# Performance work log

Measured on AMD Instinct MI355X. Metric: run time of the kernel, lower is better.

Reference implementation:

```python
import jax, jax.numpy as jnp
import numpy as np

B, C, CI, H, W = 4, 64, 32, 96, 96  # batch, in_channels, inter_channels, spatial
EPS = 1e-5


def conv1x1(x, w, b):
    # x: [B,Cin,H,W], w: [Cout,Cin], b: [Cout]
    return jnp.einsum('bchw,oc->bohw', x, w) + b[None, :, None, None]


def maxpool2(x):
    b, c, h, w = x.shape
    return x.reshape(b, c, h // 2, 2, w // 2, 2).max(axis=(3, 5))


def setup_inputs() -> dict:
    key = jax.random.key(0)
    ks = jax.random.split(key, 12)
    s = 0.05  # keep unscaled attention logits in a sane range
    return {
        'x': jax.random.normal(ks[0], (B, C, H, W), jnp.float32),
        'feature': jax.random.normal(ks[1], (B, CI, H, W), jnp.float32),
        'g_w': jax.random.normal(ks[2], (C, C), jnp.float32) * s,
        'g_b': jax.random.normal(ks[3], (C,), jnp.float32) * s,
        'theta_w': jax.random.normal(ks[4], (C, C), jnp.float32) * s,
        'theta_b': jax.random.normal(ks[5], (C,), jnp.float32) * s,
        'phi_w': jax.random.normal(ks[6], (C, CI), jnp.float32) * s,
        'phi_b': jax.random.normal(ks[7], (C,), jnp.float32) * s,
        'W_w': jax.random.normal(ks[8], (CI, C), jnp.float32) * s,
        'W_b': jax.random.normal(ks[9], (CI,), jnp.float32) * s,
        'bn_gamma': jax.random.normal(ks[10], (CI,), jnp.float32) * s + 1.0,
        'bn_beta': jax.random.normal(ks[11], (CI,), jnp.float32) * s,
    }


def reference(x, feature, g_w, g_b, theta_w, theta_b, phi_w, phi_b, W_w, W_b, bn_gamma, bn_beta):
    b = x.shape[0]
    # g branch: conv1x1 then 2x2 maxpool -> [B, M, C]
    g_x = maxpool2(conv1x1(x, g_w, g_b)).reshape(b, C, -1).transpose(0, 2, 1)
    # theta: conv1x1 -> [B, N, C]
    theta_x = conv1x1(x, theta_w, theta_b).reshape(b, C, -1).transpose(0, 2, 1)
    # phi on `feature` (inter_channels -> in_channels) then maxpool -> [B, C, M]
    phi_f = maxpool2(conv1x1(feature, phi_w, phi_b)).reshape(b, C, -1)
    # unscaled attention: [B, N, M]
    f = jnp.einsum('bnc,bcm->bnm', theta_x, phi_f)
    f_div_C = jax.nn.softmax(f, axis=-1)
    y = jnp.einsum('bnm,bmc->bnc', f_div_C, g_x)  # [B, N, C]
    y = y.transpose(0, 2, 1).reshape(x.shape)
    z = y + x
    # W: conv1x1 (C -> CI) + BatchNorm2d (training mode, batch stats)
    z = conv1x1(z, W_w, W_b)
    mean = z.mean(axis=(0, 2, 3), keepdims=True)
    var = z.var(axis=(0, 2, 3), keepdims=True)
    z = (z - mean) * jax.lax.rsqrt(var + EPS)
    z = z * bn_gamma[None, :, None, None] + bn_beta[None, :, None, None]
    return z
```

## Files before the change

kernel.cpp:

```cpp
#include <hip/hip_runtime.h>
#include <hip/hip_bf16.h>

typedef __attribute__((ext_vector_type(8))) short short8;
typedef __attribute__((ext_vector_type(4))) float f32x4;
typedef __attribute__((ext_vector_type(4))) _Float16 half4;
typedef __attribute__((ext_vector_type(8))) _Float16 half8;

#define NB 4
#define NN 9216
#define NM 2304

__device__ inline unsigned pk2(float a, float b) {
  __hip_bfloat16 ha = __float2bfloat16(a), hb = __float2bfloat16(b);
  return (unsigned)*(unsigned short*)&ha | ((unsigned)*(unsigned short*)&hb << 16);
}
__device__ inline short8 pack8(const float* v) {
  short8 s;
#pragma unroll
  for (int j = 0; j < 8; ++j) { __hip_bfloat16 h = __float2bfloat16(v[j]); s[j] = *(short*)&h; }
  return s;
}
__device__ inline short8 ldw8(const float* p) {
  float tmp[8];
  *(float4*)&tmp[0] = *(const float4*)p;
  *(float4*)&tmp[4] = *(const float4*)(p + 4);
  return pack8(tmp);
}

__global__ __launch_bounds__(256) void conv_pool_k(
    const float* __restrict__ x, const float* __restrict__ feat,
    const float* __restrict__ tw, const float* __restrict__ tbi,
    const float* __restrict__ gw, const float* __restrict__ gbi,
    const float* __restrict__ pw, const float* __restrict__ pbi,
    __hip_bfloat16* __restrict__ Theta, _Float16* __restrict__ Gcm,
    __hip_bfloat16* __restrict__ PhiT, float* __restrict__ psum) {
  int t = threadIdx.x, wv = t >> 6, lane = t & 63, l15 = lane & 15, q = lane >> 4;
  int b = blockIdx.y, bx = blockIdx.x;
  if (bx == 0 && b == 0 && t < 64) psum[t] = 0.f;
  int jt = bx % 6, rp = bx / 6;
  int i0 = rp * 2, j0 = jt * 16;
  int ntop = i0 * 96 + j0;
  int ot = wv;

  short8 wt[2], wg[2], wp1;
#pragma unroll
  for (int kf = 0; kf < 2; ++kf) {
    wt[kf] = ldw8(tw + (size_t)(ot * 16 + l15) * 64 + kf * 32 + q * 8);
    wg[kf] = ldw8(gw + (size_t)(ot * 16 + l15) * 64 + kf * 32 + q * 8);
  }
  wp1 = ldw8(pw + (size_t)(ot * 16 + l15) * 32 + q * 8);

  short8 bxf[2][2], bff[2];
  {
    float tmp[8];
#pragma unroll
    for (int row = 0; row < 2; ++row) {
#pragma unroll
      for (int kf = 0; kf < 2; ++kf) {
#pragma unroll
        for (int j = 0; j < 8; ++j)
          tmp[j] = x[((size_t)b * 64 + kf * 32 + q * 8 + j) * NN + ntop + row * 96 + l15];
        bxf[row][kf] = pack8(tmp);
      }
#pragma unroll
      for (int j = 0; j < 8; ++j)
        tmp[j] = feat[((size_t)b * 32 + q * 8 + j) * NN + ntop + row * 96 + l15];
      bff[row] = pack8(tmp);
    }
  }

  int m = rp * 48 + ((j0 + l15) >> 1);
  bool em = (l15 & 1) == 0;

#pragma unroll
  for (int row = 0; row < 2; ++row) {
    f32x4 d;
#pragma unroll
    for (int r = 0; r < 4; ++r) d[r] = tbi[ot * 16 + q * 4 + r];
    d = __builtin_amdgcn_mfma_f32_16x16x32_bf16(wt[0], bxf[row][0], d, 0, 0, 0);
    d = __builtin_amdgcn_mfma_f32_16x16x32_bf16(wt[1], bxf[row][1], d, 0, 0, 0);
    size_t base = ((size_t)b * NN + ntop + row * 96 + l15) * 64 + ot * 16 + q * 4;
    *(unsigned*)(Theta + base) = pk2(d[0], d[1]);
    *(unsigned*)(Theta + base + 2) = pk2(d[2], d[3]);
  }
  {
    f32x4 d0, d1;
#pragma unroll
    for (int r = 0; r < 4; ++r) { float bb = gbi[ot * 16 + q * 4 + r]; d0[r] = bb; d1[r] = bb; }
    d0 = __builtin_amdgcn_mfma_f32_16x16x32_bf16(wg[0], bxf[0][0], d0, 0, 0, 0);
    d0 = __builtin_amdgcn_mfma_f32_16x16x32_bf16(wg[1], bxf[0][1], d0, 0, 0, 0);
    d1 = __builtin_amdgcn_mfma_f32_16x16x32_bf16(wg[0], bxf[1][0], d1, 0, 0, 0);
    d1 = __builtin_amdgcn_mfma_f32_16x16x32_bf16(wg[1], bxf[1][1], d1, 0, 0, 0);
    float h[4];
#pragma unroll
    for (int r = 0; r < 4; ++r) {
      float v = fmaxf(d0[r], d1[r]);
      h[r] = fmaxf(v, __shfl_xor(v, 1));
    }
    if (em) {
#pragma unroll
      for (int r = 0; r < 4; ++r)
        Gcm[((size_t)b * 64 + ot * 16 + q * 4 + r) * NM + m] = (_Float16)h[r];
    }
  }
  {
    f32x4 d0, d1;
#pragma unroll
    for (int r = 0; r < 4; ++r) { float bb = pbi[ot * 16 + q * 4 + r]; d0[r] = bb; d1[r] = bb; }
    d0 = __builtin_amdgcn_mfma_f32_16x16x32_bf16(wp1, bff[0], d0, 0, 0, 0);
    d1 = __builtin_amdgcn_mfma_f32_16x16x32_bf16(wp1, bff[1], d1, 0, 0, 0);
    float h[4];
#pragma unroll
    for (int r = 0; r < 4; ++r) {
      float v = fmaxf(d0[r], d1[r]);
      h[r] = fmaxf(v, __shfl_xor(v, 1));
    }
    if (em) {
      size_t base = ((size_t)b * NM + m) * 64 + ot * 16 + q * 4;
      *(unsigned*)(PhiT + base) = pk2(h[0], h[1]);
      *(unsigned*)(PhiT + base + 2) = pk2(h[2], h[3]);
    }
  }
}

__global__ __launch_bounds__(256) void attn_k(
    const __hip_bfloat16* __restrict__ Theta, const __hip_bfloat16* __restrict__ PhiT,
    const _Float16* __restrict__ Gcm, const float* __restrict__ x,
    const float* __restrict__ Ww, const float* __restrict__ Wb,
    float* __restrict__ z2, float* __restrict__ psum) {
  __shared__ union {
    struct {
      __hip_bfloat16 phis[64][72];
      _Float16 gs2[64][72];
    } s;
    __hip_bfloat16 zacc[64][72];
  } u;
  __shared__ float rs[4][64];

  int t = threadIdx.x, wv = t >> 6, lane = t & 63;
  int l15 = lane & 15, q = lane >> 4;
  int b = blockIdx.y;
  int n0 = blockIdx.x * 64, nw = n0 + wv * 16;

  short8 tb[2];
#pragma unroll
  for (int kf = 0; kf < 2; ++kf)
    tb[kf] = *(const short8*)(Theta + ((size_t)b * NN + nw + l15) * 64 + kf * 32 + q * 8);

  f32x4 acc[4];
#pragma unroll
  for (int ct = 0; ct < 4; ++ct) acc[ct] = (f32x4){0.f, 0.f, 0.f, 0.f};
  float rsum = 0.f;

  const __hip_bfloat16* phibase = PhiT + (size_t)b * NM * 64;
  const _Float16* gbase = Gcm + (size_t)b * 64 * NM;

  for (int ck = 0; ck < NM / 64; ++ck) {
    int m0 = ck * 64;
    __syncthreads();
#pragma unroll
    for (int p = 0; p < 2; ++p) {
      int idx = p * 256 + t, r = idx >> 3, seg = idx & 7;
      *(uint4*)&u.s.phis[r][seg * 8] = *(const uint4*)(phibase + (size_t)(m0 + r) * 64 + seg * 8);
    }
#pragma unroll
    for (int p = 0; p < 2; ++p) {
      int idx = p * 256 + t, c = idx >> 3, g = idx & 7;
      int pp = g >> 2, qq = g & 3;
      const _Float16* gc = gbase + (size_t)c * NM + m0 + pp * 32 + qq * 4;
      uint2 lo = *(const uint2*)gc;
      uint2 hi = *(const uint2*)(gc + 16);
      uint4 w; w.x = lo.x; w.y = lo.y; w.z = hi.x; w.w = hi.y;
      *(uint4*)&u.s.gs2[c][g * 8] = w;
    }
    __syncthreads();

    short8 pha[4][2];
#pragma unroll
    for (int tm = 0; tm < 4; ++tm)
#pragma unroll
      for (int kf = 0; kf < 2; ++kf)
        pha[tm][kf] = *(const short8*)&u.s.phis[tm * 16 + l15][kf * 32 + q * 8];
    half8 gv[4][2];
#pragma unroll
    for (int ct = 0; ct < 4; ++ct)
#pragma unroll
      for (int pp = 0; pp < 2; ++pp)
        gv[ct][pp] = *(const half8*)&u.s.gs2[ct * 16 + l15][pp * 32 + q * 8];

    half4 pa[4];
#pragma unroll
    for (int tm = 0; tm < 4; ++tm) {
      f32x4 s = (f32x4){0.f, 0.f, 0.f, 0.f};
      s = __builtin_amdgcn_mfma_f32_16x16x32_bf16(pha[tm][0], tb[0], s, 0, 0, 0);
      s = __builtin_amdgcn_mfma_f32_16x16x32_bf16(pha[tm][1], tb[1], s, 0, 0, 0);
      float e0 = __expf(s[0]), e1 = __expf(s[1]), e2 = __expf(s[2]), e3 = __expf(s[3]);
      rsum += (e0 + e1) + (e2 + e3);
      pa[tm] = (half4){(_Float16)e0, (_Float16)e1, (_Float16)e2, (_Float16)e3};
    }
#pragma unroll
    for (int ct = 0; ct < 4; ++ct)
#pragma unroll
      for (int pp = 0; pp < 2; ++pp) {
        half4 glo = __builtin_shufflevector(gv[ct][pp], gv[ct][pp], 0, 1, 2, 3);
        half4 ghi = __builtin_shufflevector(gv[ct][pp], gv[ct][pp], 4, 5, 6, 7);
        acc[ct] = __builtin_amdgcn_mfma_f32_16x16x16f16(pa[2 * pp], glo, acc[ct], 0, 0, 0);
        acc[ct] = __builtin_amdgcn_mfma_f32_16x16x16f16(pa[2 * pp + 1], ghi, acc[ct], 0, 0, 0);
      }
  }

  float v = rsum;
  v += __shfl_xor(v, 16);
  v += __shfl_xor(v, 32);
  float rinv = 1.0f / v;
  float riv[4];
#pragma unroll
  for (int r = 0; r < 4; ++r) riv[r] = __shfl(rinv, q * 4 + r);

  __syncthreads();

#pragma unroll
  for (int ct = 0; ct < 4; ++ct) {
#pragma unroll
    for (int r = 0; r < 4; ++r) {
      float xv = x[((size_t)b * 64 + ct * 16 + l15) * NN + nw + q * 4 + r];
      u.zacc[wv * 16 + q * 4 + r][ct * 16 + l15] =
          __float2bfloat16(acc[ct][r] * riv[r] + xv);
    }
  }
  __syncthreads();

  short8 wbf[2][2];
#pragma unroll
  for (int ot = 0; ot < 2; ++ot)
#pragma unroll
    for (int kf = 0; kf < 2; ++kf)
      wbf[ot][kf] = ldw8(Ww + (size_t)(ot * 16 + l15) * 64 + kf * 32 + q * 8);
  short8 za0 = *(const short8*)&u.zacc[wv * 16 + l15][q * 8];
  short8 za1 = *(const short8*)&u.zacc[wv * 16 + l15][32 + q * 8];

  f32x4 dd[2];
#pragma unroll
  for (int ot = 0; ot < 2; ++ot) {
    float bias = Wb[ot * 16 + l15];
    f32x4 d = (f32x4){bias, bias, bias, bias};
    d = __builtin_amdgcn_mfma_f32_16x16x32_bf16(za0, wbf[ot][0], d, 0, 0, 0);
    d = __builtin_amdgcn_mfma_f32_16x16x32_bf16(za1, wbf[ot][1], d, 0, 0, 0);
#pragma unroll
    for (int r = 0; r < 4; ++r)
      z2[((size_t)b * NN + nw + q * 4 + r) * 32 + ot * 16 + l15] = d[r];
    dd[ot] = d;
  }

#pragma unroll
  for (int ot = 0; ot < 2; ++ot) {
    float ps = (dd[ot][0] + dd[ot][1]) + (dd[ot][2] + dd[ot][3]);
    float ps2 = dd[ot][0] * dd[ot][0] + dd[ot][1] * dd[ot][1] +
                dd[ot][2] * dd[ot][2] + dd[ot][3] * dd[ot][3];
    ps += __shfl_xor(ps, 16);  ps += __shfl_xor(ps, 32);
    ps2 += __shfl_xor(ps2, 16); ps2 += __shfl_xor(ps2, 32);
    if (lane < 16) {
      rs[wv][ot * 16 + lane] = ps;
      rs[wv][32 + ot * 16 + lane] = ps2;
    }
  }
  __syncthreads();
  if (t < 64) {
    float tot = rs[0][t] + rs[1][t] + rs[2][t] + rs[3][t];
    atomicAdd(&psum[t], tot);
  }
}

__global__ __launch_bounds__(256) void bn_apply(
    const float* __restrict__ z2, const float* __restrict__ psum,
    const float* __restrict__ gamma, const float* __restrict__ beta,
    float* __restrict__ out) {
  __shared__ float ssl[64];
  __shared__ float zt[32][65];
  int t = threadIdx.x, b = blockIdx.y, n0 = blockIdx.x * 64;
  if (t < 32) {
    const float inv = 1.0f / (float)(NB * NN);
    float mean = psum[t] * inv;
    float var = psum[32 + t] * inv - mean * mean;
    float sc = gamma[t] * rsqrtf(var + 1e-5f);
    ssl[t] = sc;
    ssl[32 + t] = beta[t] - mean * sc;
  }
#pragma unroll
  for (int it = 0; it < 2; ++it) {
    int idx = it * 256 + t, r = idx >> 3, seg = idx & 7;
    float4 vv = *(const float4*)(z2 + ((size_t)b * NN + n0 + r) * 32 + seg * 4);
    zt[seg * 4 + 0][r] = vv.x; zt[seg * 4 + 1][r] = vv.y;
    zt[seg * 4 + 2][r] = vv.z; zt[seg * 4 + 3][r] = vv.w;
  }
  __syncthreads();
  int o = t >> 3, nseg = t & 7;
  float sc = ssl[o], sh = ssl[32 + o];
  float4 a, c;
  a.x = zt[o][nseg * 8 + 0] * sc + sh; a.y = zt[o][nseg * 8 + 1] * sc + sh;
  a.z = zt[o][nseg * 8 + 2] * sc + sh; a.w = zt[o][nseg * 8 + 3] * sc + sh;
  c.x = zt[o][nseg * 8 + 4] * sc + sh; c.y = zt[o][nseg * 8 + 5] * sc + sh;
  c.z = zt[o][nseg * 8 + 6] * sc + sh; c.w = zt[o][nseg * 8 + 7] * sc + sh;
  float* po = out + ((size_t)b * 32 + o) * NN + n0 + nseg * 8;
  *(float4*)po = a;
  *(float4*)(po + 4) = c;
}

extern "C" void kernel_launch(void* const* d_in, const int* in_sizes, int n_in,
                              void* d_out, int out_size, void* d_ws, size_t ws_size,
                              hipStream_t stream) {
  const float* x       = (const float*)d_in[0];
  const float* feature = (const float*)d_in[1];
  const float* g_w     = (const float*)d_in[2];
  const float* g_b     = (const float*)d_in[3];
  const float* theta_w = (const float*)d_in[4];
  const float* theta_b = (const float*)d_in[5];
  const float* phi_w   = (const float*)d_in[6];
  const float* phi_b   = (const float*)d_in[7];
  const float* W_w     = (const float*)d_in[8];
  const float* W_b     = (const float*)d_in[9];
  const float* bn_g    = (const float*)d_in[10];
  const float* bn_b    = (const float*)d_in[11];

  char* ws = (char*)d_ws;
  __hip_bfloat16* Theta = (__hip_bfloat16*)(ws);
  _Float16*       Gcm   = (_Float16*)(ws + 4718592);
  __hip_bfloat16* PhiT  = (__hip_bfloat16*)(ws + 5898240);
  float*          z2    = (float*)(ws + 7077888);
  float*          psum  = (float*)(ws + 11796480);

  conv_pool_k<<<dim3(288, NB), dim3(256), 0, stream>>>(
      x, feature, theta_w, theta_b, g_w, g_b, phi_w, phi_b, Theta, Gcm, PhiT, psum);
  attn_k<<<dim3(144, NB), dim3(256), 0, stream>>>(
      Theta, PhiT, Gcm, x, W_w, W_b, z2, psum);
  bn_apply<<<dim3(144, NB), dim3(256), 0, stream>>>(
      z2, psum, bn_g, bn_b, (float*)d_out);
}
```

Measured before the change: 157.9 us.

## Split attention keys across waves and stage conv inputs through LDS

```diff
diff --git a/kernel.cpp b/kernel.cpp
--- a/kernel.cpp
+++ b/kernel.cpp
@@ -4,7 +4,6 @@
 typedef __attribute__((ext_vector_type(8))) short short8;
 typedef __attribute__((ext_vector_type(4))) float f32x4;
 typedef __attribute__((ext_vector_type(4))) _Float16 half4;
-typedef __attribute__((ext_vector_type(8))) _Float16 half8;
 
 #define NB 4
 #define NN 9216
@@ -13,6 +12,9 @@
 __device__ inline unsigned pk2(float a, float b) {
   __hip_bfloat16 ha = __float2bfloat16(a), hb = __float2bfloat16(b);
   return (unsigned)*(unsigned short*)&ha | ((unsigned)*(unsigned short*)&hb << 16);
+}
+__device__ inline float ubf(unsigned u) {
+  unsigned v = u << 16; return *(float*)&v;
 }
 __device__ inline short8 pack8(const float* v) {
   short8 s;
@@ -27,20 +29,42 @@
   return pack8(tmp);
 }
 
-__global__ __launch_bounds__(256) void conv_pool_k(
+__global__ __launch_bounds__(256, 3) void conv_pool_k(
     const float* __restrict__ x, const float* __restrict__ feat,
     const float* __restrict__ tw, const float* __restrict__ tbi,
     const float* __restrict__ gw, const float* __restrict__ gbi,
     const float* __restrict__ pw, const float* __restrict__ pbi,
     __hip_bfloat16* __restrict__ Theta, _Float16* __restrict__ Gcm,
     __hip_bfloat16* __restrict__ PhiT, float* __restrict__ psum) {
+  __shared__ float xs[64][68];
+  __shared__ float fs[64][36];
   int t = threadIdx.x, wv = t >> 6, lane = t & 63, l15 = lane & 15, q = lane >> 4;
   int b = blockIdx.y, bx = blockIdx.x;
   if (bx == 0 && b == 0 && t < 64) psum[t] = 0.f;
-  int jt = bx % 6, rp = bx / 6;
-  int i0 = rp * 2, j0 = jt * 16;
-  int ntop = i0 * 96 + j0;
+  int jt = bx % 3, rp = bx / 3;
+  int i0 = rp * 2, j0 = jt * 32;
   int ot = wv;
+
+  {
+#pragma unroll
+    for (int p = 0; p < 4; ++p) {
+      int idx = p * 256 + t;
+      int c = idx >> 4, s = idx & 15;
+      int row = s >> 3, cl = (s & 7) * 4;
+      float4 v = *(const float4*)(x + ((size_t)b * 64 + c) * NN + (i0 + row) * 96 + j0 + cl);
+      int nl = row * 32 + cl;
+      xs[nl][c] = v.x; xs[nl + 1][c] = v.y; xs[nl + 2][c] = v.z; xs[nl + 3][c] = v.w;
+    }
+#pragma unroll
+    for (int p = 0; p < 2; ++p) {
+      int idx = p * 256 + t;
+      int c = idx >> 4, s = idx & 15;
+      int row = s >> 3, cl = (s & 7) * 4;
+      float4 v = *(const float4*)(feat + ((size_t)b * 32 + c) * NN + (i0 + row) * 96 + j0 + cl);
+      int nl = row * 32 + cl;
+      fs[nl][c] = v.x; fs[nl + 1][c] = v.y; fs[nl + 2][c] = v.z; fs[nl + 3][c] = v.w;
+    }
+  }
 
   short8 wt[2], wg[2], wp1;
 #pragma unroll
@@ -50,47 +74,49 @@
   }
   wp1 = ldw8(pw + (size_t)(ot * 16 + l15) * 32 + q * 8);
 
-  short8 bxf[2][2], bff[2];
+  __syncthreads();
+
+  short8 bxf[4][2], bff[4];
   {
     float tmp[8];
 #pragma unroll
-    for (int row = 0; row < 2; ++row) {
+    for (int tl = 0; tl < 4; ++tl) {
 #pragma unroll
       for (int kf = 0; kf < 2; ++kf) {
-#pragma unroll
-        for (int j = 0; j < 8; ++j)
-          tmp[j] = x[((size_t)b * 64 + kf * 32 + q * 8 + j) * NN + ntop + row * 96 + l15];
-        bxf[row][kf] = pack8(tmp);
+        *(float4*)&tmp[0] = *(float4*)&xs[tl * 16 + l15][kf * 32 + q * 8];
+        *(float4*)&tmp[4] = *(float4*)&xs[tl * 16 + l15][kf * 32 + q * 8 + 4];
+        bxf[tl][kf] = pack8(tmp);
       }
-#pragma unroll
-      for (int j = 0; j < 8; ++j)
-        tmp[j] = feat[((size_t)b * 32 + q * 8 + j) * NN + ntop + row * 96 + l15];
-      bff[row] = pack8(tmp);
-    }
-  }
-
-  int m = rp * 48 + ((j0 + l15) >> 1);
-  bool em = (l15 & 1) == 0;
-
-#pragma unroll
-  for (int row = 0; row < 2; ++row) {
+      *(float4*)&tmp[0] = *(float4*)&fs[tl * 16 + l15][q * 8];
+      *(float4*)&tmp[4] = *(float4*)&fs[tl * 16 + l15][q * 8 + 4];
+      bff[tl] = pack8(tmp);
+    }
+  }
+
+#pragma unroll
+  for (int tl = 0; tl < 4; ++tl) {
     f32x4 d;
 #pragma unroll
     for (int r = 0; r < 4; ++r) d[r] = tbi[ot * 16 + q * 4 + r];
-    d = __builtin_amdgcn_mfma_f32_16x16x32_bf16(wt[0], bxf[row][0], d, 0, 0, 0);
-    d = __builtin_amdgcn_mfma_f32_16x16x32_bf16(wt[1], bxf[row][1], d, 0, 0, 0);
-    size_t base = ((size_t)b * NN + ntop + row * 96 + l15) * 64 + ot * 16 + q * 4;
+    d = __builtin_amdgcn_mfma_f32_16x16x32_bf16(wt[0], bxf[tl][0], d, 0, 0, 0);
+    d = __builtin_amdgcn_mfma_f32_16x16x32_bf16(wt[1], bxf[tl][1], d, 0, 0, 0);
+    int n = (i0 + (tl >> 1)) * 96 + j0 + (tl & 1) * 16 + l15;
+    size_t base = ((size_t)b * NN + n) * 64 + ot * 16 + q * 4;
     *(unsigned*)(Theta + base) = pk2(d[0], d[1]);
     *(unsigned*)(Theta + base + 2) = pk2(d[2], d[3]);
   }
-  {
+
+  int mrow = rp * 48 + jt * 16;
+  bool em = (l15 & 1) == 0;
+#pragma unroll
+  for (int ch = 0; ch < 2; ++ch) {
     f32x4 d0, d1;
 #pragma unroll
     for (int r = 0; r < 4; ++r) { float bb = gbi[ot * 16 + q * 4 + r]; d0[r] = bb; d1[r] = bb; }
-    d0 = __builtin_amdgcn_mfma_f32_16x16x32_bf16(wg[0], bxf[0][0], d0, 0, 0, 0);
-    d0 = __builtin_amdgcn_mfma_f32_16x16x32_bf16(wg[1], bxf[0][1], d0, 0, 0, 0);
-    d1 = __builtin_amdgcn_mfma_f32_16x16x32_bf16(wg[0], bxf[1][0], d1, 0, 0, 0);
-    d1 = __builtin_amdgcn_mfma_f32_16x16x32_bf16(wg[1], bxf[1][1], d1, 0, 0, 0);
+    d0 = __builtin_amdgcn_mfma_f32_16x16x32_bf16(wg[0], bxf[ch][0], d0, 0, 0, 0);
+    d0 = __builtin_amdgcn_mfma_f32_16x16x32_bf16(wg[1], bxf[ch][1], d0, 0, 0, 0);
+    d1 = __builtin_amdgcn_mfma_f32_16x16x32_bf16(wg[0], bxf[ch + 2][0], d1, 0, 0, 0);
+    d1 = __builtin_amdgcn_mfma_f32_16x16x32_bf16(wg[1], bxf[ch + 2][1], d1, 0, 0, 0);
     float h[4];
 #pragma unroll
     for (int r = 0; r < 4; ++r) {
@@ -98,17 +124,19 @@
       h[r] = fmaxf(v, __shfl_xor(v, 1));
     }
     if (em) {
+      int m = mrow + ch * 8 + (l15 >> 1);
 #pragma unroll
       for (int r = 0; r < 4; ++r)
         Gcm[((size_t)b * 64 + ot * 16 + q * 4 + r) * NM + m] = (_Float16)h[r];
     }
   }
-  {
+#pragma unroll
+  for (int ch = 0; ch < 2; ++ch) {
     f32x4 d0, d1;
 #pragma unroll
     for (int r = 0; r < 4; ++r) { float bb = pbi[ot * 16 + q * 4 + r]; d0[r] = bb; d1[r] = bb; }
-    d0 = __builtin_amdgcn_mfma_f32_16x16x32_bf16(wp1, bff[0], d0, 0, 0, 0);
-    d1 = __builtin_amdgcn_mfma_f32_16x16x32_bf16(wp1, bff[1], d1, 0, 0, 0);
+    d0 = __builtin_amdgcn_mfma_f32_16x16x32_bf16(wp1, bff[ch], d0, 0, 0, 0);
+    d1 = __builtin_amdgcn_mfma_f32_16x16x32_bf16(wp1, bff[ch + 2], d1, 0, 0, 0);
     float h[4];
 #pragma unroll
     for (int r = 0; r < 4; ++r) {
@@ -116,6 +144,7 @@
       h[r] = fmaxf(v, __shfl_xor(v, 1));
     }
     if (em) {
+      int m = mrow + ch * 8 + (l15 >> 1);
       size_t base = ((size_t)b * NM + m) * 64 + ot * 16 + q * 4;
       *(unsigned*)(PhiT + base) = pk2(h[0], h[1]);
       *(unsigned*)(PhiT + base + 2) = pk2(h[2], h[3]);
@@ -123,34 +152,35 @@
   }
 }
 
-__global__ __launch_bounds__(256) void attn_k(
+__global__ __launch_bounds__(256, 3) void attn_k(
     const __hip_bfloat16* __restrict__ Theta, const __hip_bfloat16* __restrict__ PhiT,
     const _Float16* __restrict__ Gcm, const float* __restrict__ x,
     const float* __restrict__ Ww, const float* __restrict__ Wb,
     float* __restrict__ z2, float* __restrict__ psum) {
   __shared__ union {
-    struct {
-      __hip_bfloat16 phis[64][72];
-      _Float16 gs2[64][72];
-    } s;
-    __hip_bfloat16 zacc[64][72];
+    struct { __hip_bfloat16 phis[64][72]; _Float16 gs[64][72]; } st;
+    struct { __hip_bfloat16 zpart[4][64][68]; __hip_bfloat16 zacc[64][72]; } ep;
   } u;
   __shared__ float rs[4][64];
 
   int t = threadIdx.x, wv = t >> 6, lane = t & 63;
   int l15 = lane & 15, q = lane >> 4;
   int b = blockIdx.y;
-  int n0 = blockIdx.x * 64, nw = n0 + wv * 16;
-
-  short8 tb[2];
-#pragma unroll
-  for (int kf = 0; kf < 2; ++kf)
-    tb[kf] = *(const short8*)(Theta + ((size_t)b * NN + nw + l15) * 64 + kf * 32 + q * 8);
-
-  f32x4 acc[4];
-#pragma unroll
-  for (int ct = 0; ct < 4; ++ct) acc[ct] = (f32x4){0.f, 0.f, 0.f, 0.f};
-  float rsum = 0.f;
+  int n0 = blockIdx.x * 64;
+
+  short8 tb[4][2];
+#pragma unroll
+  for (int nt = 0; nt < 4; ++nt)
+#pragma unroll
+    for (int kf = 0; kf < 2; ++kf)
+      tb[nt][kf] = *(const short8*)(Theta + ((size_t)b * NN + n0 + nt * 16 + l15) * 64 + kf * 32 + q * 8);
+
+  f32x4 acc[4][4];
+#pragma unroll
+  for (int nt = 0; nt < 4; ++nt)
+#pragma unroll
+    for (int ct = 0; ct < 4; ++ct) acc[nt][ct] = (f32x4){0.f, 0.f, 0.f, 0.f};
+  float rsum[4] = {0.f, 0.f, 0.f, 0.f};
 
   const __hip_bfloat16* phibase = PhiT + (size_t)b * NM * 64;
   const _Float16* gbase = Gcm + (size_t)b * 64 * NM;
@@ -161,83 +191,98 @@
 #pragma unroll
     for (int p = 0; p < 2; ++p) {
       int idx = p * 256 + t, r = idx >> 3, seg = idx & 7;
-      *(uint4*)&u.s.phis[r][seg * 8] = *(const uint4*)(phibase + (size_t)(m0 + r) * 64 + seg * 8);
+      *(uint4*)&u.st.phis[r][seg * 8] = *(const uint4*)(phibase + (size_t)(m0 + r) * 64 + seg * 8);
     }
 #pragma unroll
     for (int p = 0; p < 2; ++p) {
-      int idx = p * 256 + t, c = idx >> 3, g = idx & 7;
-      int pp = g >> 2, qq = g & 3;
-      const _Float16* gc = gbase + (size_t)c * NM + m0 + pp * 32 + qq * 4;
-      uint2 lo = *(const uint2*)gc;
-      uint2 hi = *(const uint2*)(gc + 16);
-      uint4 w; w.x = lo.x; w.y = lo.y; w.z = hi.x; w.w = hi.y;
-      *(uint4*)&u.s.gs2[c][g * 8] = w;
+      int idx = p * 256 + t, c = idx >> 3, seg = idx & 7;
+      *(uint4*)&u.st.gs[c][seg * 8] = *(const uint4*)(gbase + (size_t)c * NM + m0 + seg * 8);
     }
     __syncthreads();
 
-    short8 pha[4][2];
-#pragma unroll
-    for (int tm = 0; tm < 4; ++tm)
-#pragma unroll
-      for (int kf = 0; kf < 2; ++kf)
-        pha[tm][kf] = *(const short8*)&u.s.phis[tm * 16 + l15][kf * 32 + q * 8];
-    half8 gv[4][2];
+    short8 pha[2];
+#pragma unroll
+    for (int kf = 0; kf < 2; ++kf)
+      pha[kf] = *(const short8*)&u.st.phis[wv * 16 + l15][kf * 32 + q * 8];
+    half4 gv[4];
 #pragma unroll
     for (int ct = 0; ct < 4; ++ct)
-#pragma unroll
-      for (int pp = 0; pp < 2; ++pp)
-        gv[ct][pp] = *(const half8*)&u.s.gs2[ct * 16 + l15][pp * 32 + q * 8];
+      gv[ct] = *(const half4*)&u.st.gs[ct * 16 + l15][wv * 16 + q * 4];
 
     half4 pa[4];
 #pragma unroll
-    for (int tm = 0; tm < 4; ++tm) {
+    for (int nt = 0; nt < 4; ++nt) {
       f32x4 s = (f32x4){0.f, 0.f, 0.f, 0.f};
-      s = __builtin_amdgcn_mfma_f32_16x16x32_bf16(pha[tm][0], tb[0], s, 0, 0, 0);
-      s = __builtin_amdgcn_mfma_f32_16x16x32_bf16(pha[tm][1], tb[1], s, 0, 0, 0);
+      s = __builtin_amdgcn_mfma_f32_16x16x32_bf16(pha[0], tb[nt][0], s, 0, 0, 0);
+      s = __builtin_amdgcn_mfma_f32_16x16x32_bf16(pha[1], tb[nt][1], s, 0, 0, 0);
       float e0 = __expf(s[0]), e1 = __expf(s[1]), e2 = __expf(s[2]), e3 = __expf(s[3]);
-      rsum += (e0 + e1) + (e2 + e3);
-      pa[tm] = (half4){(_Float16)e0, (_Float16)e1, (_Float16)e2, (_Float16)e3};
-    }
+      rsum[nt] += (e0 + e1) + (e2 + e3);
+      pa[nt] = (half4){(_Float16)e0, (_Float16)e1, (_Float16)e2, (_Float16)e3};
+    }
+#pragma unroll
+    for (int nt = 0; nt < 4; ++nt)
+#pragma unroll
+      for (int ct = 0; ct < 4; ++ct)
+        acc[nt][ct] = __builtin_amdgcn_mfma_f32_16x16x16f16(pa[nt], gv[ct], acc[nt][ct], 0, 0, 0);
+  }
+
+#pragma unroll
+  for (int nt = 0; nt < 4; ++nt) {
+    float v = rsum[nt];
+    v += __shfl_xor(v, 16);
+    v += __shfl_xor(v, 32);
+    if (lane < 16) rs[wv][nt * 16 + lane] = v;
+  }
+  __syncthreads();
+
+#pragma unroll
+  for (int nt = 0; nt < 4; ++nt)
 #pragma unroll
     for (int ct = 0; ct < 4; ++ct)
 #pragma unroll
-      for (int pp = 0; pp < 2; ++pp) {
-        half4 glo = __builtin_shufflevector(gv[ct][pp], gv[ct][pp], 0, 1, 2, 3);
-        half4 ghi = __builtin_shufflevector(gv[ct][pp], gv[ct][pp], 4, 5, 6, 7);
-        acc[ct] = __builtin_amdgcn_mfma_f32_16x16x16f16(pa[2 * pp], glo, acc[ct], 0, 0, 0);
-        acc[ct] = __builtin_amdgcn_mfma_f32_16x16x16f16(pa[2 * pp + 1], ghi, acc[ct], 0, 0, 0);
+      for (int r = 0; r < 4; ++r)
+        u.ep.zpart[wv][nt * 16 + q * 4 + r][ct * 16 + l15] = __float2bfloat16(acc[nt][ct][r]);
+  __syncthreads();
+
+  {
+    int row = wv * 16 + l15;
+    float tot = rs[0][row] + rs[1][row] + rs[2][row] + rs[3][row];
+    float rinv = 1.0f / tot;
+    float ys[16];
+#pragma unroll
+    for (int j4 = 0; j4 < 4; ++j4) {
+      uint2 p0 = *(const uint2*)&u.ep.zpart[0][row][q * 16 + j4 * 4];
+      ys[j4 * 4 + 0] = ubf(p0.x & 0xffffu); ys[j4 * 4 + 1] = ubf(p0.x >> 16);
+      ys[j4 * 4 + 2] = ubf(p0.y & 0xffffu); ys[j4 * 4 + 3] = ubf(p0.y >> 16);
+    }
+#pragma unroll
+    for (int wvv = 1; wvv < 4; ++wvv) {
+#pragma unroll
+      for (int j4 = 0; j4 < 4; ++j4) {
+        uint2 p0 = *(const uint2*)&u.ep.zpart[wvv][row][q * 16 + j4 * 4];
+        ys[j4 * 4 + 0] += ubf(p0.x & 0xffffu); ys[j4 * 4 + 1] += ubf(p0.x >> 16);
+        ys[j4 * 4 + 2] += ubf(p0.y & 0xffffu); ys[j4 * 4 + 3] += ubf(p0.y >> 16);
       }
-  }
-
-  float v = rsum;
-  v += __shfl_xor(v, 16);
-  v += __shfl_xor(v, 32);
-  float rinv = 1.0f / v;
-  float riv[4];
-#pragma unroll
-  for (int r = 0; r < 4; ++r) riv[r] = __shfl(rinv, q * 4 + r);
-
-  __syncthreads();
-
-#pragma unroll
-  for (int ct = 0; ct < 4; ++ct) {
-#pragma unroll
-    for (int r = 0; r < 4; ++r) {
-      float xv = x[((size_t)b * 64 + ct * 16 + l15) * NN + nw + q * 4 + r];
-      u.zacc[wv * 16 + q * 4 + r][ct * 16 + l15] =
-          __float2bfloat16(acc[ct][r] * riv[r] + xv);
-    }
-  }
-  __syncthreads();
-
+    }
+    float z1[16];
+#pragma unroll
+    for (int i = 0; i < 16; ++i)
+      z1[i] = ys[i] * rinv + x[((size_t)b * 64 + q * 16 + i) * NN + n0 + row];
+#pragma unroll
+    for (int i2 = 0; i2 < 8; ++i2)
+      *(unsigned*)&u.ep.zacc[row][q * 16 + 2 * i2] = pk2(z1[2 * i2], z1[2 * i2 + 1]);
+  }
+  __syncthreads();
+
+  int nw = n0 + wv * 16;
   short8 wbf[2][2];
 #pragma unroll
   for (int ot = 0; ot < 2; ++ot)
 #pragma unroll
     for (int kf = 0; kf < 2; ++kf)
       wbf[ot][kf] = ldw8(Ww + (size_t)(ot * 16 + l15) * 64 + kf * 32 + q * 8);
-  short8 za0 = *(const short8*)&u.zacc[wv * 16 + l15][q * 8];
-  short8 za1 = *(const short8*)&u.zacc[wv * 16 + l15][32 + q * 8];
+  short8 za0 = *(const short8*)&u.ep.zacc[wv * 16 + l15][q * 8];
+  short8 za1 = *(const short8*)&u.ep.zacc[wv * 16 + l15][32 + q * 8];
 
   f32x4 dd[2];
 #pragma unroll
@@ -252,6 +297,7 @@
     dd[ot] = d;
   }
 
+  __syncthreads();
 #pragma unroll
   for (int ot = 0; ot < 2; ++ot) {
     float ps = (dd[ot][0] + dd[ot][1]) + (dd[ot][2] + dd[ot][3]);
@@ -329,7 +375,7 @@
   float*          z2    = (float*)(ws + 7077888);
   float*          psum  = (float*)(ws + 11796480);
 
-  conv_pool_k<<<dim3(288, NB), dim3(256), 0, stream>>>(
+  conv_pool_k<<<dim3(144, NB), dim3(256), 0, stream>>>(
       x, feature, theta_w, theta_b, g_w, g_b, phi_w, phi_b, Theta, Gcm, PhiT, psum);
   attn_k<<<dim3(144, NB), dim3(256), 0, stream>>>(
       Theta, PhiT, Gcm, x, W_w, W_b, z2, psum);
```

Measured after the change: 148.8 us. 5.8% less time.
